# Performance work log

Hardware: AMD Instinct MI355X
Metric: run time of the kernel (lower is better)

## Reference

```python
import jax, jax.numpy as jnp
import numpy as np

LN_EPS = 1e-5

def _layernorm(x, gamma, beta):
    mu = jnp.mean(x, axis=-1, keepdims=True)
    var = jnp.mean(jnp.square(x - mu), axis=-1, keepdims=True)
    return (x - mu) * jax.lax.rsqrt(var + LN_EPS) * gamma + beta

def setup_inputs() -> dict:
    key = jax.random.key(0)
    ks = jax.random.split(key, 10)
    d_model, outdim = 1024, 512
    n_support, n_queries = 8192, 8192
    s = 1.0 / np.sqrt(d_model)
    return {
        "support_set": jax.random.normal(ks[0], (n_support, d_model), jnp.float32),
        "queries": jax.random.normal(ks[1], (n_queries, d_model), jnp.float32),
        "Wq": jax.random.uniform(ks[2], (outdim, d_model), jnp.float32, -s, s),
        "bq": jax.random.uniform(ks[3], (outdim,), jnp.float32, -s, s),
        "Wk": jax.random.uniform(ks[4], (outdim, d_model), jnp.float32, -s, s),
        "bk": jax.random.uniform(ks[5], (outdim,), jnp.float32, -s, s),
        "Wv": jax.random.uniform(ks[6], (outdim, d_model), jnp.float32, -s, s),
        "bv": jax.random.uniform(ks[7], (outdim,), jnp.float32, -s, s),
        "ln_gamma": jnp.ones((outdim,), jnp.float32),
        "ln_beta": jnp.zeros((outdim,), jnp.float32),
    }

def reference(support_set, queries, Wq, bq, Wk, bk, Wv, bv, ln_gamma, ln_beta):
    outdim = Wq.shape[0]
    # V projections
    support_vs = support_set @ Wv.T + bv            # [Ns, O]
    q_prototype = queries @ Wv.T + bv               # [Nq, O]
    # QK projections, shared LayerNorm (norm_k applied to both)
    support_ks = _layernorm(support_set @ Wk.T + bk, ln_gamma, ln_beta)  # [Ns, O]
    queries_qs = _layernorm(queries @ Wq.T + bq, ln_gamma, ln_beta)     # [Nq, O]
    # scaled scores + softmax over support axis (dim=1)
    scores = (queries_qs @ support_ks.T) / jnp.sqrt(jnp.float32(outdim))  # [Nq, Ns]
    affinity = jax.nn.softmax(scores, axis=1)
    class_prototype = affinity @ support_vs         # [Nq, O]
    return (q_prototype, class_prototype)
```

## Files before the change

kernel.cpp:

```cpp
#include <hip/hip_runtime.h>
#include <hip/hip_bf16.h>

typedef __attribute__((ext_vector_type(8))) short bf16x8;
typedef __attribute__((ext_vector_type(4))) float f32x4;
typedef __attribute__((ext_vector_type(4))) short short4_t;
typedef __attribute__((ext_vector_type(8))) short short8_t;
typedef __attribute__((ext_vector_type(4))) float float4_t;

#define MFMA16(a, b, c) __builtin_amdgcn_mfma_f32_16x16x32_bf16((a), (b), (c), 0, 0, 0)

__device__ __forceinline__ unsigned short f2bf(float f) {
    unsigned u = __builtin_bit_cast(unsigned, f);
    u += 0x7fffu + ((u >> 16) & 1u);
    return (unsigned short)(u >> 16);
}

__device__ __forceinline__ short4_t pack4(float4_t v) {
    short4_t r;
    r[0] = (short)f2bf(v[0]);
    r[1] = (short)f2bf(v[1]);
    r[2] = (short)f2bf(v[2]);
    r[3] = (short)f2bf(v[3]);
    return r;
}

__device__ __forceinline__ void gload_lds16(const void* g, void* l) {
    __builtin_amdgcn_global_load_lds(
        (const __attribute__((address_space(1))) unsigned int*)g,
        (__attribute__((address_space(3))) unsigned int*)l, 16, 0, 0);
}

__global__ __launch_bounds__(256) void cast_kernel(
    const float* __restrict__ support, const float* __restrict__ queries,
    const float* __restrict__ Wq, const float* __restrict__ Wk,
    const float* __restrict__ Wv,
    unsigned short* __restrict__ sb, unsigned short* __restrict__ qb,
    unsigned short* __restrict__ wqb, unsigned short* __restrict__ wkb,
    unsigned short* __restrict__ wvb)
{
    const size_t e = ((size_t)blockIdx.x * 256 + threadIdx.x) * 8;
    const float* src; unsigned short* dst; size_t off;
    if (e < 8388608)       { src = support; dst = sb;  off = e; }
    else if (e < 16777216) { src = queries; dst = qb;  off = e - 8388608; }
    else if (e < 17301504) { src = Wq;      dst = wqb; off = e - 16777216; }
    else if (e < 17825792) { src = Wk;      dst = wkb; off = e - 17301504; }
    else                   { src = Wv;      dst = wvb; off = e - 17825792; }
    float4_t a = *(const float4_t*)(src + off);
    float4_t b = *(const float4_t*)(src + off + 4);
    short4_t lo = pack4(a), hi = pack4(b);
    short8_t o;
    o[0] = lo[0]; o[1] = lo[1]; o[2] = lo[2]; o[3] = lo[3];
    o[4] = hi[0]; o[5] = hi[1]; o[6] = hi[2]; o[7] = hi[3];
    *(short8_t*)(dst + off) = o;
}

__global__ __launch_bounds__(512, 2) void proj_v_kernel(
    const unsigned short* __restrict__ sb, const unsigned short* __restrict__ qb,
    const unsigned short* __restrict__ wvb, const float* __restrict__ bv,
    float* __restrict__ q_proto, unsigned short* __restrict__ VsT)
{
    const int mode = blockIdx.x >> 7;
    const int rem = blockIdx.x & 127;
    const int rowbase = (rem >> 1) * 128;
    const int colbase = (rem & 1) * 256;
    const unsigned short* A = mode ? sb : qb;

    const int t = threadIdx.x;
    const int w = t >> 6, l = t & 63, lg = l >> 4, ll = l & 15;
    const int wr = w & 1, wc = w >> 1;
    const int sr = l >> 3, su = l & 7;

    __shared__ unsigned short Alds[2][128][64];
    __shared__ unsigned short Blds[2][256][64];

    f32x4 acc[4][4];
    #pragma unroll
    for (int i = 0; i < 4; ++i)
        #pragma unroll
        for (int j = 0; j < 4; ++j) acc[i][j] = (f32x4){0.f, 0.f, 0.f, 0.f};

    #define PV_STAGE(buf, kt)                                                   \
        {                                                                       \
            const int kc = (kt) * 64;                                           \
            _Pragma("unroll")                                                   \
            for (int g = 0; g < 2; ++g) {                                       \
                const int r0 = w * 16 + g * 8, row = r0 + sr;                   \
                gload_lds16(A + (size_t)(rowbase + row) * 1024 + kc             \
                                + ((su ^ (row & 7)) << 3),                      \
                            &Alds[buf][r0][0]);                                 \
            }                                                                   \
            _Pragma("unroll")                                                   \
            for (int g = 0; g < 4; ++g) {                                       \
                const int r0 = w * 32 + g * 8, row = r0 + sr;                   \
                gload_lds16(wvb + (size_t)(colbase + row) * 1024 + kc           \
                                + ((su ^ (row & 7)) << 3),                      \
                            &Blds[buf][r0][0]);                                 \
            }                                                                   \
        }

    PV_STAGE(0, 0)
    __syncthreads();

    for (int kt = 0; kt < 16; ++kt) {
        const int cur = kt & 1;
        if (kt < 15) PV_STAGE(cur ^ 1, kt + 1)
        #pragma unroll
        for (int ks = 0; ks < 2; ++ks) {
            const int u = ((ks * 4 + lg) ^ (ll & 7)) * 8;
            bf16x8 af[4], bfr[4];
            #pragma unroll
            for (int mf = 0; mf < 4; ++mf)
                af[mf] = *(const bf16x8*)&Alds[cur][wr * 64 + mf * 16 + ll][u];
            #pragma unroll
            for (int nf = 0; nf < 4; ++nf)
                bfr[nf] = *(const bf16x8*)&Blds[cur][wc * 64 + nf * 16 + ll][u];
            #pragma unroll
            for (int mf = 0; mf < 4; ++mf)
                #pragma unroll
                for (int nf = 0; nf < 4; ++nf)
                    acc[mf][nf] = MFMA16(af[mf], bfr[nf], acc[mf][nf]);
        }
        __syncthreads();
    }
    #undef PV_STAGE

    float bvv[4];
    #pragma unroll
    for (int nf = 0; nf < 4; ++nf) bvv[nf] = bv[colbase + wc * 64 + nf * 16 + ll];

    if (mode == 0) {
        #pragma unroll
        for (int mf = 0; mf < 4; ++mf)
            #pragma unroll
            for (int r = 0; r < 4; ++r) {
                const size_t row = rowbase + wr * 64 + mf * 16 + lg * 4 + r;
                #pragma unroll
                for (int nf = 0; nf < 4; ++nf)
                    q_proto[row * 512 + colbase + wc * 64 + nf * 16 + ll] = acc[mf][nf][r] + bvv[nf];
            }
    } else {
        #pragma unroll
        for (int mf = 0; mf < 4; ++mf)
            #pragma unroll
            for (int nf = 0; nf < 4; ++nf) {
                float4_t pv = {acc[mf][nf][0] + bvv[nf], acc[mf][nf][1] + bvv[nf],
                               acc[mf][nf][2] + bvv[nf], acc[mf][nf][3] + bvv[nf]};
                const size_t col = colbase + wc * 64 + nf * 16 + ll;
                *(short4_t*)&VsT[col * 8192 + rowbase + wr * 64 + mf * 16 + lg * 4] = pack4(pv);
            }
    }
}

__global__ __launch_bounds__(512, 2) void proj_ln_kernel(
    const unsigned short* __restrict__ sb, const unsigned short* __restrict__ qb,
    const unsigned short* __restrict__ wkb, const float* __restrict__ bk,
    const unsigned short* __restrict__ wqb, const float* __restrict__ bq,
    const float* __restrict__ gamma, const float* __restrict__ beta,
    unsigned short* __restrict__ Ks, unsigned short* __restrict__ Qs)
{
    const int mode = blockIdx.x >> 7;
    const int rowbase = (blockIdx.x & 127) * 64;
    const unsigned short* A = mode ? qb : sb;
    const unsigned short* W = mode ? wqb : wkb;
    const float* bias = mode ? bq : bk;
    unsigned short* dst = mode ? Qs : Ks;

    const int t = threadIdx.x;
    const int w = t >> 6, l = t & 63, lg = l >> 4, ll = l & 15;
    const int sr = l >> 3, su = l & 7;

    __shared__ unsigned short Alds[2][64][64];
    __shared__ unsigned short Blds[2][512][64];
    __shared__ float red[8][64][2];
    __shared__ float stats[64][2];

    f32x4 acc[4][4];
    #pragma unroll
    for (int i = 0; i < 4; ++i)
        #pragma unroll
        for (int j = 0; j < 4; ++j) acc[i][j] = (f32x4){0.f, 0.f, 0.f, 0.f};

    #define LN_STAGE(buf, kt)                                                   \
        {                                                                       \
            const int kc = (kt) * 64;                                           \
            {                                                                   \
                const int r0 = w * 8, row = r0 + sr;                            \
                gload_lds16(A + (size_t)(rowbase + row) * 1024 + kc             \
                                + ((su ^ (row & 7)) << 3),                      \
                            &Alds[buf][r0][0]);                                 \
            }                                                                   \
            _Pragma("unroll")                                                   \
            for (int g = 0; g < 8; ++g) {                                       \
                const int r0 = w * 64 + g * 8, row = r0 + sr;                   \
                gload_lds16(W + (size_t)row * 1024 + kc                         \
                                + ((su ^ (row & 7)) << 3),                      \
                            &Blds[buf][r0][0]);                                 \
            }                                                                   \
        }

    LN_STAGE(0, 0)
    __syncthreads();

    for (int kt = 0; kt < 16; ++kt) {
        const int cur = kt & 1;
        if (kt < 15) LN_STAGE(cur ^ 1, kt + 1)
        #pragma unroll
        for (int ks = 0; ks < 2; ++ks) {
            const int u = ((ks * 4 + lg) ^ (ll & 7)) * 8;
            bf16x8 af[4], bfr[4];
            #pragma unroll
            for (int mf = 0; mf < 4; ++mf)
                af[mf] = *(const bf16x8*)&Alds[cur][mf * 16 + ll][u];
            #pragma unroll
            for (int nf = 0; nf < 4; ++nf)
                bfr[nf] = *(const bf16x8*)&Blds[cur][w * 64 + nf * 16 + ll][u];
            #pragma unroll
            for (int mf = 0; mf < 4; ++mf)
                #pragma unroll
                for (int nf = 0; nf < 4; ++nf)
                    acc[mf][nf] = MFMA16(af[mf], bfr[nf], acc[mf][nf]);
        }
        __syncthreads();
    }
    #undef LN_STAGE

    float bvv[4];
    #pragma unroll
    for (int nf = 0; nf < 4; ++nf) bvv[nf] = bias[w * 64 + nf * 16 + ll];

    float v[4][4][4];
    #pragma unroll
    for (int mf = 0; mf < 4; ++mf)
        #pragma unroll
        for (int nf = 0; nf < 4; ++nf)
            #pragma unroll
            for (int r = 0; r < 4; ++r)
                v[mf][nf][r] = acc[mf][nf][r] + bvv[nf];

    #pragma unroll
    for (int mf = 0; mf < 4; ++mf)
        #pragma unroll
        for (int r = 0; r < 4; ++r) {
            float s = 0.f, q = 0.f;
            #pragma unroll
            for (int nf = 0; nf < 4; ++nf) { s += v[mf][nf][r]; q += v[mf][nf][r] * v[mf][nf][r]; }
            #pragma unroll
            for (int d = 1; d < 16; d <<= 1) { s += __shfl_xor(s, d); q += __shfl_xor(q, d); }
            if (ll == 0) {
                red[w][mf * 16 + lg * 4 + r][0] = s;
                red[w][mf * 16 + lg * 4 + r][1] = q;
            }
        }
    __syncthreads();
    if (t < 64) {
        float S = 0.f, Q = 0.f;
        #pragma unroll
        for (int w2 = 0; w2 < 8; ++w2) { S += red[w2][t][0]; Q += red[w2][t][1]; }
        const float mu = S * (1.f / 512.f);
        const float var = Q * (1.f / 512.f) - mu * mu;
        stats[t][0] = mu;
        stats[t][1] = rsqrtf(var + 1e-5f);
    }
    __syncthreads();
    float gv[4], bev[4];
    #pragma unroll
    for (int nf = 0; nf < 4; ++nf) {
        gv[nf] = gamma[w * 64 + nf * 16 + ll];
        bev[nf] = beta[w * 64 + nf * 16 + ll];
    }
    #pragma unroll
    for (int mf = 0; mf < 4; ++mf)
        #pragma unroll
        for (int r = 0; r < 4; ++r) {
            const int row = mf * 16 + lg * 4 + r;
            const float mu = stats[row][0], rs = stats[row][1];
            #pragma unroll
            for (int nf = 0; nf < 4; ++nf) {
                const float o = (v[mf][nf][r] - mu) * rs * gv[nf] + bev[nf];
                dst[(size_t)(rowbase + row) * 512 + w * 64 + nf * 16 + ll] = f2bf(o);
            }
        }
}

__global__ __launch_bounds__(512, 2) void attn_kernel(
    const unsigned short* __restrict__ Qs, const unsigned short* __restrict__ Ks,
    const unsigned short* __restrict__ VsT,
    float* __restrict__ Opart, float* __restrict__ lpart)
{
    const int bid = blockIdx.x;
    const int sp = (bid & 7) >> 2;
    const int qb = (bid >> 3) * 4 + (bid & 3);
    const int qbase = qb * 64;
    const int kv0 = sp * 4096;
    const int t = threadIdx.x;
    const int w = t >> 6, l = t & 63, lg = l >> 4, ll = l & 15;
    const int wq = w & 3, wk = w >> 2;

    __shared__ unsigned short Klds[2][64][512];
    __shared__ unsigned short Plds[2][64][64];
    __shared__ float lsum[2][64];

    bf16x8 qf[16];
    {
        const unsigned short* qrow = Qs + (size_t)(qbase + wq * 16 + ll) * 512 + lg * 8;
        #pragma unroll
        for (int ks = 0; ks < 16; ++ks)
            qf[ks] = *(const bf16x8*)(qrow + ks * 32);
    }

    f32x4 oacc[4][4];
    #pragma unroll
    for (int i = 0; i < 4; ++i)
        #pragma unroll
        for (int j = 0; j < 4; ++j) oacc[i][j] = (f32x4){0.f, 0.f, 0.f, 0.f};
    float lrun[4] = {0.f, 0.f, 0.f, 0.f};
    const float scale = 0.044194173824159216f;

    #define K_STAGE(buf, kvt)                                                   \
        {                                                                       \
            _Pragma("unroll")                                                   \
            for (int rr = 0; rr < 8; ++rr) {                                    \
                const int r = w * 8 + rr;                                       \
                gload_lds16(Ks + (size_t)((kvt) + r) * 512 + ((l ^ (r & 7)) << 3), \
                            &Klds[buf][r][0]);                                  \
            }                                                                   \
        }

    K_STAGE(0, kv0)
    __syncthreads();
    K_STAGE(1, kv0 + 64)

    {
        f32x4 s0 = (f32x4){0.f, 0.f, 0.f, 0.f}, s1 = (f32x4){0.f, 0.f, 0.f, 0.f};
        #pragma unroll
        for (int j = 0; j < 16; ++j) {
            const int u = ((j * 4 + lg) ^ (ll & 7)) * 8;
            bf16x8 ka = *(const bf16x8*)&Klds[0][wk * 32 + ll][u];
            bf16x8 kb = *(const bf16x8*)&Klds[0][wk * 32 + 16 + ll][u];
            s0 = MFMA16(qf[j], ka, s0);
            s1 = MFMA16(qf[j], kb, s1);
        }
        #pragma unroll
        for (int r = 0; r < 4; ++r) {
            const int row = wq * 16 + lg * 4 + r;
            const int swz = (row >> 1) & 7;
            const float p0 = __expf(s0[r] * scale);
            const float p1 = __expf(s1[r] * scale);
            const int c0 = wk * 32 + ll, c1 = c0 + 16;
            Plds[0][row][(((c0 >> 3) ^ swz) << 3) + (c0 & 7)] = f2bf(p0);
            Plds[0][row][(((c1 >> 3) ^ swz) << 3) + (c1 & 7)] = f2bf(p1);
            lrun[r] += p0 + p1;
        }
    }
    __syncthreads();

    for (int it = 0; it < 63; ++it) {
        const int cur = it & 1, nxt = cur ^ 1;
        const int kvb = kv0 + it * 64;

        bf16x8 vf[2][4];
        #pragma unroll
        for (int ks2 = 0; ks2 < 2; ++ks2)
            #pragma unroll
            for (int nf = 0; nf < 4; ++nf)
                vf[ks2][nf] = *(const bf16x8*)(VsT + (size_t)(w * 64 + nf * 16 + ll) * 8192
                                               + kvb + ks2 * 32 + lg * 8);
        if (it < 62) K_STAGE(cur, kvb + 128)

        f32x4 s0 = (f32x4){0.f, 0.f, 0.f, 0.f}, s1 = (f32x4){0.f, 0.f, 0.f, 0.f};
        bf16x8 pf;
        __builtin_amdgcn_s_setprio(1);
        #pragma unroll
        for (int j = 0; j < 16; ++j) {
            const int u = ((j * 4 + lg) ^ (ll & 7)) * 8;
            bf16x8 ka = *(const bf16x8*)&Klds[nxt][wk * 32 + ll][u];
            bf16x8 kb = *(const bf16x8*)&Klds[nxt][wk * 32 + 16 + ll][u];
            s0 = MFMA16(qf[j], ka, s0);
            s1 = MFMA16(qf[j], kb, s1);
            #pragma unroll
            for (int s = 0; s < 2; ++s) {
                const int f = 2 * j + s;
                const int ks2 = f >> 4, mf = (f >> 2) & 3, nf = f & 3;
                if (nf == 0) {
                    const int row = mf * 16 + ll;
                    const int unit = (ks2 * 4 + lg) ^ ((row >> 1) & 7);
                    pf = *(const bf16x8*)&Plds[cur][row][unit * 8];
                }
                oacc[mf][nf] = MFMA16(pf, vf[ks2][nf], oacc[mf][nf]);
            }
        }
        __builtin_amdgcn_s_setprio(0);

        #pragma unroll
        for (int r = 0; r < 4; ++r) {
            const int row = wq * 16 + lg * 4 + r;
            const int swz = (row >> 1) & 7;
            const float p0 = __expf(s0[r] * scale);
            const float p1 = __expf(s1[r] * scale);
            const int c0 = wk * 32 + ll, c1 = c0 + 16;
            Plds[nxt][row][(((c0 >> 3) ^ swz) << 3) + (c0 & 7)] = f2bf(p0);
            Plds[nxt][row][(((c1 >> 3) ^ swz) << 3) + (c1 & 7)] = f2bf(p1);
            lrun[r] += p0 + p1;
        }
        __syncthreads();
    }
    #undef K_STAGE

    {
        const int kvb = kv0 + 63 * 64;
        #pragma unroll
        for (int ks2 = 0; ks2 < 2; ++ks2) {
            bf16x8 vf[4];
            #pragma unroll
            for (int nf = 0; nf < 4; ++nf)
                vf[nf] = *(const bf16x8*)(VsT + (size_t)(w * 64 + nf * 16 + ll) * 8192
                                          + kvb + ks2 * 32 + lg * 8);
            #pragma unroll
            for (int mf = 0; mf < 4; ++mf) {
                const int row = mf * 16 + ll;
                const int unit = (ks2 * 4 + lg) ^ ((row >> 1) & 7);
                bf16x8 pf = *(const bf16x8*)&Plds[1][row][unit * 8];
                #pragma unroll
                for (int nf = 0; nf < 4; ++nf)
                    oacc[mf][nf] = MFMA16(pf, vf[nf], oacc[mf][nf]);
            }
        }
    }

    const size_t obase = (size_t)sp * 8192 + qbase;
    #pragma unroll
    for (int mf = 0; mf < 4; ++mf)
        #pragma unroll
        for (int r = 0; r < 4; ++r) {
            const size_t row = obase + mf * 16 + lg * 4 + r;
            #pragma unroll
            for (int nf = 0; nf < 4; ++nf)
                Opart[row * 512 + w * 64 + nf * 16 + ll] = oacc[mf][nf][r];
        }

    #pragma unroll
    for (int r = 0; r < 4; ++r) {
        float val = lrun[r];
        #pragma unroll
        for (int d = 1; d < 16; d <<= 1) val += __shfl_xor(val, d);
        if (ll == 0)
            lsum[wk][wq * 16 + lg * 4 + r] = val;
    }
    __syncthreads();
    if (t < 64)
        lpart[(size_t)sp * 8192 + qbase + t] = lsum[0][t] + lsum[1][t];
}

__global__ __launch_bounds__(256) void merge_kernel(
    const float* __restrict__ Opart, const float* __restrict__ lpart,
    float* __restrict__ out2)
{
    const int idx = blockIdx.x * 256 + threadIdx.x;
    const int q = idx >> 7;
    const int c = (idx & 127) * 4;
    float4_t a = {0.f, 0.f, 0.f, 0.f};
    float ls = 0.f;
    #pragma unroll
    for (int s = 0; s < 2; ++s) {
        float4_t vv = *(const float4_t*)(Opart + ((size_t)s * 8192 + q) * 512 + c);
        a += vv;
        ls += lpart[s * 8192 + q];
    }
    const float inv = 1.f / ls;
    *(float4_t*)(out2 + (size_t)q * 512 + c) = a * inv;
}

extern "C" void kernel_launch(void* const* d_in, const int* in_sizes, int n_in,
                              void* d_out, int out_size, void* d_ws, size_t ws_size,
                              hipStream_t stream)
{
    const float* support = (const float*)d_in[0];
    const float* queries = (const float*)d_in[1];
    const float* Wq = (const float*)d_in[2];
    const float* bq = (const float*)d_in[3];
    const float* Wk = (const float*)d_in[4];
    const float* bk = (const float*)d_in[5];
    const float* Wv = (const float*)d_in[6];
    const float* bv = (const float*)d_in[7];
    const float* gamma = (const float*)d_in[8];
    const float* beta = (const float*)d_in[9];

    float* out = (float*)d_out;
    float* q_proto = out;
    float* out2 = out + (size_t)8192 * 512;

    char* ws = (char*)d_ws;
    unsigned short* Qs  = (unsigned short*)(ws);
    unsigned short* Ks  = (unsigned short*)(ws + ((size_t)8 << 20));
    unsigned short* VsT = (unsigned short*)(ws + ((size_t)16 << 20));
    unsigned short* sb  = (unsigned short*)(ws + ((size_t)24 << 20));
    unsigned short* qbuf= (unsigned short*)(ws + ((size_t)40 << 20));
    unsigned short* wqb = (unsigned short*)(ws + ((size_t)56 << 20));
    unsigned short* wkb = (unsigned short*)(ws + ((size_t)57 << 20));
    unsigned short* wvb = (unsigned short*)(ws + ((size_t)58 << 20));
    float* Opart = (float*)(ws + ((size_t)24 << 20));
    float* lpart = (float*)(ws + ((size_t)59 << 20));

    cast_kernel<<<8960, 256, 0, stream>>>(support, queries, Wq, Wk, Wv,
                                          sb, qbuf, wqb, wkb, wvb);
    proj_v_kernel<<<256, 512, 0, stream>>>(sb, qbuf, wvb, bv, q_proto, VsT);
    proj_ln_kernel<<<256, 512, 0, stream>>>(sb, qbuf, wkb, bk, wqb, bq,
                                            gamma, beta, Ks, Qs);
    attn_kernel<<<256, 512, 0, stream>>>(Qs, Ks, VsT, Opart, lpart);
    merge_kernel<<<4096, 256, 0, stream>>>(Opart, lpart, out2);
}
```

Baseline: 337.6 us.

## Restructure attention loop into 32-key tiles with 4-deep K ring buffer

Replaces the software-pipelined attention loop, which interleaved the QK of the next tile with the PV of the current tile over 64-key tiles, with a simpler per-iteration sequence over 32-key tiles. K is staged through a 4-slot LDS ring and waited on with an explicit partial vmcnt barrier, so K loads stay in flight across iterations. LDS use drops, but the loop now has twice as many iterations and barriers and no longer overlaps QK MFMAs with PV MFMAs. That may expose latency around the P exchange.

```diff
diff --git a/kernel.cpp b/kernel.cpp
--- a/kernel.cpp
+++ b/kernel.cpp
@@ -29,6 +29,13 @@
         (const __attribute__((address_space(1))) unsigned int*)g,
         (__attribute__((address_space(3))) unsigned int*)l, 16, 0, 0);
 }
+
+#define BARRIER_VM(N)                                                        \
+    do {                                                                     \
+        asm volatile("s_waitcnt vmcnt(" #N ") lgkmcnt(0)" ::: "memory");     \
+        __builtin_amdgcn_sched_barrier(0);                                   \
+        __builtin_amdgcn_s_barrier();                                        \
+    } while (0)
 
 __global__ __launch_bounds__(256) void cast_kernel(
     const float* __restrict__ support, const float* __restrict__ queries,
@@ -296,8 +303,8 @@
     const int w = t >> 6, l = t & 63, lg = l >> 4, ll = l & 15;
     const int wq = w & 3, wk = w >> 2;
 
-    __shared__ unsigned short Klds[2][64][512];
-    __shared__ unsigned short Plds[2][64][64];
+    __shared__ unsigned short Klds[4][32][512];
+    __shared__ unsigned short Plds[2][64][32];
     __shared__ float lsum[2][64];
 
     bf16x8 qf[16];
@@ -319,113 +326,64 @@
     #define K_STAGE(buf, kvt)                                                   \
         {                                                                       \
             _Pragma("unroll")                                                   \
-            for (int rr = 0; rr < 8; ++rr) {                                    \
-                const int r = w * 8 + rr;                                       \
+            for (int rr = 0; rr < 4; ++rr) {                                    \
+                const int r = w * 4 + rr;                                       \
                 gload_lds16(Ks + (size_t)((kvt) + r) * 512 + ((l ^ (r & 7)) << 3), \
                             &Klds[buf][r][0]);                                  \
             }                                                                   \
         }
 
     K_STAGE(0, kv0)
-    __syncthreads();
-    K_STAGE(1, kv0 + 64)
-
-    {
-        f32x4 s0 = (f32x4){0.f, 0.f, 0.f, 0.f}, s1 = (f32x4){0.f, 0.f, 0.f, 0.f};
-        #pragma unroll
-        for (int j = 0; j < 16; ++j) {
-            const int u = ((j * 4 + lg) ^ (ll & 7)) * 8;
-            bf16x8 ka = *(const bf16x8*)&Klds[0][wk * 32 + ll][u];
-            bf16x8 kb = *(const bf16x8*)&Klds[0][wk * 32 + 16 + ll][u];
-            s0 = MFMA16(qf[j], ka, s0);
-            s1 = MFMA16(qf[j], kb, s1);
-        }
+    K_STAGE(1, kv0 + 32)
+    BARRIER_VM(4);
+
+    for (int it = 0; it < 128; ++it) {
+        const int cur = it & 3, pcur = it & 1;
+        const int kvb = kv0 + it * 32;
+
+        if (it < 126) K_STAGE((it + 2) & 3, kvb + 64)
+
+        bf16x8 vf[4];
+        #pragma unroll
+        for (int nf = 0; nf < 4; ++nf)
+            vf[nf] = *(const bf16x8*)(VsT + (size_t)(w * 64 + nf * 16 + ll) * 8192
+                                      + kvb + lg * 8);
+
+        f32x4 sacc = (f32x4){0.f, 0.f, 0.f, 0.f};
+        __builtin_amdgcn_s_setprio(1);
+        #pragma unroll
+        for (int ks = 0; ks < 16; ++ks) {
+            const int u = ((ks * 4 + lg) ^ (ll & 7)) * 8;
+            bf16x8 kf = *(const bf16x8*)&Klds[cur][wk * 16 + ll][u];
+            sacc = MFMA16(qf[ks], kf, sacc);
+        }
+        __builtin_amdgcn_s_setprio(0);
+
         #pragma unroll
         for (int r = 0; r < 4; ++r) {
             const int row = wq * 16 + lg * 4 + r;
-            const int swz = (row >> 1) & 7;
-            const float p0 = __expf(s0[r] * scale);
-            const float p1 = __expf(s1[r] * scale);
-            const int c0 = wk * 32 + ll, c1 = c0 + 16;
-            Plds[0][row][(((c0 >> 3) ^ swz) << 3) + (c0 & 7)] = f2bf(p0);
-            Plds[0][row][(((c1 >> 3) ^ swz) << 3) + (c1 & 7)] = f2bf(p1);
-            lrun[r] += p0 + p1;
-        }
-    }
-    __syncthreads();
-
-    for (int it = 0; it < 63; ++it) {
-        const int cur = it & 1, nxt = cur ^ 1;
-        const int kvb = kv0 + it * 64;
-
-        bf16x8 vf[2][4];
-        #pragma unroll
-        for (int ks2 = 0; ks2 < 2; ++ks2)
+            const float p = __expf(sacc[r] * scale);
+            const int col = wk * 16 + ll;
+            const int unit = (col >> 3) ^ ((row >> 1) & 3);
+            Plds[pcur][row][unit * 8 + (col & 7)] = f2bf(p);
+            lrun[r] += p;
+        }
+
+        BARRIER_VM(8);
+
+        __builtin_amdgcn_s_setprio(1);
+        #pragma unroll
+        for (int mf = 0; mf < 4; ++mf) {
+            const int row = mf * 16 + ll;
+            const int unit = lg ^ ((row >> 1) & 3);
+            bf16x8 pf = *(const bf16x8*)&Plds[pcur][row][unit * 8];
             #pragma unroll
             for (int nf = 0; nf < 4; ++nf)
-                vf[ks2][nf] = *(const bf16x8*)(VsT + (size_t)(w * 64 + nf * 16 + ll) * 8192
-                                               + kvb + ks2 * 32 + lg * 8);
-        if (it < 62) K_STAGE(cur, kvb + 128)
-
-        f32x4 s0 = (f32x4){0.f, 0.f, 0.f, 0.f}, s1 = (f32x4){0.f, 0.f, 0.f, 0.f};
-        bf16x8 pf;
-        __builtin_amdgcn_s_setprio(1);
-        #pragma unroll
-        for (int j = 0; j < 16; ++j) {
-            const int u = ((j * 4 + lg) ^ (ll & 7)) * 8;
-            bf16x8 ka = *(const bf16x8*)&Klds[nxt][wk * 32 + ll][u];
-            bf16x8 kb = *(const bf16x8*)&Klds[nxt][wk * 32 + 16 + ll][u];
-            s0 = MFMA16(qf[j], ka, s0);
-            s1 = MFMA16(qf[j], kb, s1);
-            #pragma unroll
-            for (int s = 0; s < 2; ++s) {
-                const int f = 2 * j + s;
-                const int ks2 = f >> 4, mf = (f >> 2) & 3, nf = f & 3;
-                if (nf == 0) {
-                    const int row = mf * 16 + ll;
-                    const int unit = (ks2 * 4 + lg) ^ ((row >> 1) & 7);
-                    pf = *(const bf16x8*)&Plds[cur][row][unit * 8];
-                }
-                oacc[mf][nf] = MFMA16(pf, vf[ks2][nf], oacc[mf][nf]);
-            }
+                oacc[mf][nf] = MFMA16(pf, vf[nf], oacc[mf][nf]);
         }
         __builtin_amdgcn_s_setprio(0);
-
-        #pragma unroll
-        for (int r = 0; r < 4; ++r) {
-            const int row = wq * 16 + lg * 4 + r;
-            const int swz = (row >> 1) & 7;
-            const float p0 = __expf(s0[r] * scale);
-            const float p1 = __expf(s1[r] * scale);
-            const int c0 = wk * 32 + ll, c1 = c0 + 16;
-            Plds[nxt][row][(((c0 >> 3) ^ swz) << 3) + (c0 & 7)] = f2bf(p0);
-            Plds[nxt][row][(((c1 >> 3) ^ swz) << 3) + (c1 & 7)] = f2bf(p1);
-            lrun[r] += p0 + p1;
-        }
-        __syncthreads();
     }
     #undef K_STAGE
-
-    {
-        const int kvb = kv0 + 63 * 64;
-        #pragma unroll
-        for (int ks2 = 0; ks2 < 2; ++ks2) {
-            bf16x8 vf[4];
-            #pragma unroll
-            for (int nf = 0; nf < 4; ++nf)
-                vf[nf] = *(const bf16x8*)(VsT + (size_t)(w * 64 + nf * 16 + ll) * 8192
-                                          + kvb + ks2 * 32 + lg * 8);
-            #pragma unroll
-            for (int mf = 0; mf < 4; ++mf) {
-                const int row = mf * 16 + ll;
-                const int unit = (ks2 * 4 + lg) ^ ((row >> 1) & 7);
-                bf16x8 pf = *(const bf16x8*)&Plds[1][row][unit * 8];
-                #pragma unroll
-                for (int nf = 0; nf < 4; ++nf)
-                    oacc[mf][nf] = MFMA16(pf, vf[nf], oacc[mf][nf]);
-            }
-        }
-    }
 
     const size_t obase = (size_t)sp * 8192 + qbase;
     #pragma unroll
```

New measurement: 354.5 us. 5.0% more time.
